# Kernel tuning notes

Hardware: AMD Instinct MI355X
Metric: run time of the kernel (lower is better)

## Reference

```python
import jax, jax.numpy as jnp
import numpy as np

H = 16  # num_heads


def setup_inputs() -> dict:
    key = jax.random.key(0)
    ks = jax.random.split(key, 12)
    b, n, c, T = 4, 1024, 512, 4096

    def lin_w(k, out_d, in_d):
        return jax.random.normal(k, (out_d, in_d), jnp.float32) * (1.0 / np.sqrt(in_d))

    return {
        "feat": jax.random.normal(ks[0], (b, n, c), jnp.float32),
        "member_idx": jax.random.randint(ks[1], (b, n), 0, n),
        "cluster_mask": jnp.ones((b, n), jnp.int32),
        "pe_idx": jax.random.randint(ks[2], (b, n, n), 0, T),
        "global_attn": 1,
        "pre_table": jax.random.normal(ks[3], (T, 5), jnp.float32),
        "q_w": lin_w(ks[4], c, c), "q_b": jnp.zeros((c,), jnp.float32),
        "kv_w": lin_w(ks[5], 2 * c, c), "kv_b": jnp.zeros((2 * c,), jnp.float32),
        "pe_w": lin_w(ks[6], H, 5), "pe_b": jnp.zeros((H,), jnp.float32),
        "blank_k": jax.random.normal(ks[7], (c,), jnp.float32) * 0.2,
        "blank_v": jax.random.normal(ks[8], (c,), jnp.float32) * 0.2,
        "proj_w": lin_w(ks[9], c, c), "proj_b": jnp.zeros((c,), jnp.float32),
    }


def reference(feat, member_idx, cluster_mask, pe_idx, global_attn, pre_table,
              q_w, q_b, kv_w, kv_b, pe_w, pe_b, blank_k, blank_v, proj_w, proj_b):
    # global_attn path only (member_idx / cluster_mask unused in this branch)
    b, n, c = feat.shape
    h = H
    c_ = c // h
    scale = c_ ** -0.5

    q = (feat @ q_w.T + q_b) * scale                      # [b,n,c]
    q = q.reshape(b, n, h, c_).transpose(0, 2, 1, 3)      # [b,h,n,c_]
    kv = (feat @ kv_w.T + kv_b).reshape(b, n, h, 2, c_)
    key = kv[..., 0, :].transpose(0, 2, 1, 3)             # [b,h,n,c_]
    v = kv[..., 1, :].transpose(0, 2, 1, 3)               # [b,h,n,c_]

    attn = jnp.einsum('bhqd,bhkd->bhqk', q, key)          # [b,h,n,n]

    pe_out = pre_table @ pe_w.T + pe_b                    # [T,h]
    pos = pe_out[pe_idx].transpose(0, 3, 1, 2)            # [b,h,n,n]
    attn = attn + pos

    blank = jnp.sum(q * blank_k.reshape(1, h, 1, c_), axis=-1, keepdims=True)  # [b,h,n,1]
    attn = jax.nn.softmax(jnp.concatenate([attn, blank], axis=-1), axis=-1)
    blank_attn = attn[..., -1:]                           # [b,h,n,1]
    attn = attn[..., :-1]                                 # [b,h,n,n]

    out = jnp.einsum('bhqk,bhkd->bhqd', attn, v)          # [b,h,n,c_]
    out = out + blank_attn * blank_v.reshape(1, h, 1, c_)
    out = out.transpose(0, 2, 1, 3).reshape(b, n, c)
    return out @ proj_w.T + proj_b
```

## Files before the change

kernel.cpp:

```cpp
#include <hip/hip_runtime.h>
#include <hip/hip_fp16.h>

typedef __attribute__((ext_vector_type(8))) short short8;
typedef __attribute__((ext_vector_type(8))) __bf16 bf16x8;
typedef __attribute__((ext_vector_type(4))) float f32x4;
typedef __attribute__((ext_vector_type(16))) float f32x16;

#define DEV __device__ __forceinline__

DEV unsigned short f2bf(float f) {
    unsigned int u = __float_as_uint(f);
    return (unsigned short)((u + 0x7FFFu + ((u >> 16) & 1u)) >> 16);
}
DEV float bf2f(unsigned short s) { return __uint_as_float(((unsigned int)s) << 16); }
DEV bf16x8 asbf(short8 v) { return __builtin_bit_cast(bf16x8, v); }

__global__ __launch_bounds__(256) void k_prep(const float* __restrict__ feat,
                                              const float* __restrict__ qw, const float* __restrict__ qb,
                                              const float* __restrict__ kvw, const float* __restrict__ kvb,
                                              const float* __restrict__ pew, const float* __restrict__ peb,
                                              const float* __restrict__ pret, const float* __restrict__ projw,
                                              unsigned short* __restrict__ featb,
                                              unsigned short* __restrict__ wqkv, float* __restrict__ bqkv,
                                              unsigned short* __restrict__ projwb, unsigned short* __restrict__ peG) {
    const float scale = 0.17677669529663687f;
    int i0 = blockIdx.x * 256 + threadIdx.x;
    if (i0 < 262144) {
        const float4* f4 = (const float4*)feat + (size_t)i0 * 2;
        float4 a = f4[0], c = f4[1];
        short8 o;
        o[0] = (short)f2bf(a.x); o[1] = (short)f2bf(a.y);
        o[2] = (short)f2bf(a.z); o[3] = (short)f2bf(a.w);
        o[4] = (short)f2bf(c.x); o[5] = (short)f2bf(c.y);
        o[6] = (short)f2bf(c.z); o[7] = (short)f2bf(c.w);
        ((short8*)featb)[i0] = o;
        return;
    }
    int i = i0 - 262144;
    if (i < 786432) {
        int o = i >> 9, k = i & 511;
        float v = (o < 512) ? qw[(o << 9) + k] * scale : kvw[((o - 512) << 9) + k];
        wqkv[i] = f2bf(v);
    } else if (i < 786432 + 262144) {
        int j = i - 786432;
        projwb[j] = f2bf(projw[j]);
    } else if (i < 786432 + 262144 + 1536) {
        int o = i - (786432 + 262144);
        bqkv[o] = (o < 512) ? qb[o] * scale : kvb[o - 512];
    } else if (i < 786432 + 262144 + 1536 + 65536) {
        int j = i - (786432 + 262144 + 1536);
        int t = j >> 4, h = j & 15;
        float s = peb[h];
#pragma unroll
        for (int u = 0; u < 5; u++) s += pret[t * 5 + u] * pew[h * 5 + u];
        peG[(size_t)(h >> 2) * 16384 + t * 4 + (h & 3)] =
            __builtin_bit_cast(unsigned short, __float2half(s));
    }
}

__global__ __launch_bounds__(256) void k_qkv(const unsigned short* __restrict__ A,
                                             const unsigned short* __restrict__ Bw,
                                             const float* __restrict__ bias,
                                             unsigned short* __restrict__ Qf,
                                             unsigned short* __restrict__ Kf,
                                             unsigned short* __restrict__ Vf) {
    __shared__ __align__(16) unsigned short As[128][72];
    __shared__ __align__(16) unsigned short Bs[64][72];
    int tid = threadIdx.x, lane = tid & 63, wid = tid >> 6;
    int m0 = blockIdx.y * 128, n0 = blockIdx.x * 64;
    int wm = wid >> 1, wn = wid & 1;
    f32x4 acc[4][2] = {};

    for (int k0 = 0; k0 < 512; k0 += 64) {
        {
            int row = tid >> 1, cs = (tid & 1) * 32;
            const short8* src = (const short8*)(A + (size_t)(m0 + row) * 512 + k0 + cs);
            short8* dst = (short8*)(&As[row][cs]);
            dst[0] = src[0]; dst[1] = src[1]; dst[2] = src[2]; dst[3] = src[3];
        }
        {
            int row = tid >> 2, cs = (tid & 3) * 16;
            const short8* src = (const short8*)(Bw + (size_t)(n0 + row) * 512 + k0 + cs);
            short8* dst = (short8*)(&Bs[row][cs]);
            dst[0] = src[0]; dst[1] = src[1];
        }
        __syncthreads();
#pragma unroll
        for (int kk = 0; kk < 64; kk += 32) {
            short8 a[4], b[2];
#pragma unroll
            for (int m = 0; m < 4; m++)
                a[m] = *(const short8*)(&As[wm * 64 + m * 16 + (lane & 15)][kk + ((lane >> 4) << 3)]);
#pragma unroll
            for (int n = 0; n < 2; n++)
                b[n] = *(const short8*)(&Bs[wn * 32 + n * 16 + (lane & 15)][kk + ((lane >> 4) << 3)]);
#pragma unroll
            for (int m = 0; m < 4; m++) {
#pragma unroll
                for (int n = 0; n < 2; n++)
                    acc[m][n] = __builtin_amdgcn_mfma_f32_16x16x32_bf16(asbf(a[m]), asbf(b[n]), acc[m][n], 0, 0, 0);
            }
        }
        __syncthreads();
    }
#pragma unroll
    for (int m = 0; m < 4; m++) {
#pragma unroll
        for (int n = 0; n < 2; n++) {
            int col = n0 + wn * 32 + n * 16 + (lane & 15);
            float bv = bias[col];
#pragma unroll
            for (int r = 0; r < 4; r++) {
                int row = m0 + wm * 64 + m * 16 + ((lane >> 4) << 2) + r;
                float v = acc[m][n][r] + bv;
                unsigned short bb = f2bf(v);
                int batch = row >> 10, nn = row & 1023;
                if (col < 512) {
                    int h = col >> 5, d = col & 31;
                    int bh = (batch << 4) + h;
                    int qt = nn >> 5, q5 = nn & 31;
                    int sub = d >> 4, hi2 = (d >> 3) & 1, j = d & 7;
                    Qf[((((size_t)(bh * 32 + qt) * 2 + sub) * 64) + hi2 * 32 + q5) * 8 + j] = bb;
                } else {
                    int oo = col - 512, h = oo >> 6, rem = oo & 63;
                    int bh = (batch << 4) + h;
                    int kt = nn >> 6, ks = (nn >> 5) & 1;
                    if (rem < 32) {
                        int d = rem, half = d >> 4, hi2 = (d >> 3) & 1, j = d & 7, q5 = nn & 31;
                        Kf[((((size_t)((bh * 16 + kt) * 2 + ks) * 2 + half) * 64) + hi2 * 32 + q5) * 8 + j] = bb;
                    } else {
                        int d = rem - 32, nb = nn & 31;
                        int half = nb >> 4, hi2 = (nb >> 3) & 1, j = nb & 7;
                        Vf[((((size_t)((bh * 16 + kt) * 2 + ks) * 2 + half) * 64) + hi2 * 32 + d) * 8 + j] = bb;
                    }
                }
            }
        }
    }
}

__global__ __launch_bounds__(256, 3) void k_attn(const unsigned short* __restrict__ Qf,
                                                 const unsigned short* __restrict__ Kf,
                                                 const unsigned short* __restrict__ Vf,
                                                 const int* __restrict__ pe_idx,
                                                 const unsigned short* __restrict__ peG,
                                                 const float* __restrict__ blank_k,
                                                 const float* __restrict__ blank_v,
                                                 unsigned short* __restrict__ attnO) {
    __shared__ __align__(8) unsigned short peT4[4096][4];
    __shared__ unsigned short idxT[64][34];
    __shared__ unsigned posS[4096];

    int tid = threadIdx.x, lane = tid & 63, w = tid >> 6;
    int q5 = lane & 31, hi = lane >> 5;
    int bid = blockIdx.x;
    int b = bid & 3, qt = (bid >> 2) & 31, hg = bid >> 7;
    int q0 = qt * 32;
    int head = hg * 4 + w, bh = (b << 4) + head;
    int dwsel = w >> 1, halfsel = w & 1;

    {
        const unsigned short* pg = peG + (size_t)hg * 16384;
#pragma unroll
        for (int j2 = 0; j2 < 16; j2++) {
            int r = tid + 256 * j2;
            *(uint2*)&peT4[r][0] = *(const uint2*)(pg + r * 4);
        }
    }

    int sq = tid >> 3, sk8 = (tid & 7) * 8;
    const int* pib = pe_idx + ((size_t)((b << 10) + q0 + sq)) * 1024 + sk8;

    short8 qf[2];
    float lb_, m_run, l_run;
    f32x16 accO = {};
    const f32x16 zero16 = {};

    {
        const unsigned short* qb_ = Qf + ((size_t)(bh * 32 + qt) * 2) * 512 + lane * 8;
        qf[0] = *(const short8*)(qb_);
        qf[1] = *(const short8*)(qb_ + 512);
        float dot = 0.f;
#pragma unroll
        for (int sub = 0; sub < 2; sub++) {
            const float* bk = blank_k + head * 32 + sub * 16 + hi * 8;
#pragma unroll
            for (int t = 0; t < 8; t++) dot += bf2f((unsigned short)qf[sub][t]) * bk[t];
        }
        dot += __shfl_xor(dot, 32, 64);
        lb_ = dot;
        m_run = dot;
        l_run = 1.0f;
    }

    {
        int4 a0 = *(const int4*)(pib);
        int4 a1 = *(const int4*)(pib + 4);
        idxT[sk8 + 0][sq] = (unsigned short)a0.x; idxT[sk8 + 1][sq] = (unsigned short)a0.y;
        idxT[sk8 + 2][sq] = (unsigned short)a0.z; idxT[sk8 + 3][sq] = (unsigned short)a0.w;
        idxT[sk8 + 4][sq] = (unsigned short)a1.x; idxT[sk8 + 5][sq] = (unsigned short)a1.y;
        idxT[sk8 + 6][sq] = (unsigned short)a1.z; idxT[sk8 + 7][sq] = (unsigned short)a1.w;
    }
    __syncthreads();

    for (int kt = 0; kt < 16; kt++) {
#pragma unroll
        for (int j = 0; j < 8; j++) {
            int el = tid + 256 * j;
            int idx = idxT[el >> 5][el & 31];
            uint2 pv = *(const uint2*)&peT4[idx][0];
            *(uint2*)&posS[el * 2] = pv;
        }
        __syncthreads();

        int4 n0_, n1_;
        if (kt < 15) {
            n0_ = *(const int4*)(pib + (kt + 1) * 64);
            n1_ = *(const int4*)(pib + (kt + 1) * 64 + 4);
        }

        f32x16 st[2];
#pragma unroll
        for (int ks = 0; ks < 2; ks++) {
            const unsigned short* kp = Kf + ((size_t)((bh * 16 + kt) * 2 + ks) * 2) * 512 + lane * 8;
            short8 kf0 = *(const short8*)(kp);
            short8 kf1 = *(const short8*)(kp + 512);
            st[ks] = __builtin_amdgcn_mfma_f32_32x32x16_bf16(asbf(kf0), asbf(qf[0]), zero16, 0, 0, 0);
            st[ks] = __builtin_amdgcn_mfma_f32_32x32x16_bf16(asbf(kf1), asbf(qf[1]), st[ks], 0, 0, 0);
        }
#pragma unroll
        for (int ks = 0; ks < 2; ks++) {
#pragma unroll
            for (int r = 0; r < 16; r++) {
                int kl = (r & 3) + 8 * (r >> 2) + 4 * hi + 32 * ks;
                unsigned pd = posS[(kl * 32 + q5) * 2 + dwsel];
                __half2 h2 = __builtin_bit_cast(__half2, pd);
                st[ks][r] += halfsel ? __high2float(h2) : __low2float(h2);
            }
        }
        float tm[16];
#pragma unroll
        for (int i = 0; i < 16; i++) tm[i] = fmaxf(st[0][i], st[1][i]);
#pragma unroll
        for (int i = 0; i < 8; i++) tm[i] = fmaxf(tm[i], tm[i + 8]);
#pragma unroll
        for (int i = 0; i < 4; i++) tm[i] = fmaxf(tm[i], tm[i + 4]);
        float mx = fmaxf(fmaxf(tm[0], tm[1]), fmaxf(tm[2], tm[3]));
        mx = fmaxf(mx, __shfl_xor(mx, 32, 64));
        if (!__all(mx <= m_run + 8.0f)) {
            float mn = fmaxf(m_run, mx);
            float fac = __expf(m_run - mn);
            m_run = mn;
            l_run *= fac;
#pragma unroll
            for (int r = 0; r < 16; r++) {
                int qrow = (r & 3) + 8 * (r >> 2) + 4 * hi;
                float facr = __shfl(fac, qrow, 64);
                accO[r] *= facr;
            }
        }
#pragma unroll
        for (int ks = 0; ks < 2; ks++)
#pragma unroll
            for (int r = 0; r < 16; r++)
                st[ks][r] = __expf(st[ks][r] - m_run);
        float ts[16];
#pragma unroll
        for (int i = 0; i < 16; i++) ts[i] = st[0][i] + st[1][i];
#pragma unroll
        for (int i = 0; i < 8; i++) ts[i] += ts[i + 8];
#pragma unroll
        for (int i = 0; i < 4; i++) ts[i] += ts[i + 4];
        float sum = (ts[0] + ts[1]) + (ts[2] + ts[3]);
        sum += __shfl_xor(sum, 32, 64);
        l_run += sum;
#pragma unroll
        for (int ks = 0; ks < 2; ks++) {
            unsigned pk_[8];
#pragma unroll
            for (int i = 0; i < 8; i++) {
                float plo = st[ks][2 * i], phi = st[ks][2 * i + 1];
                asm("v_cvt_pk_bf16_f32 %0, %1, %2" : "=v"(pk_[i]) : "v"(plo), "v"(phi));
            }
            asm("v_permlane32_swap_b32 %0, %1" : "+v"(pk_[0]), "+v"(pk_[2]));
            asm("v_permlane32_swap_b32 %0, %1" : "+v"(pk_[1]), "+v"(pk_[3]));
            asm("v_permlane32_swap_b32 %0, %1" : "+v"(pk_[4]), "+v"(pk_[6]));
            asm("v_permlane32_swap_b32 %0, %1" : "+v"(pk_[5]), "+v"(pk_[7]));
            uint4 u0 = {pk_[0], pk_[1], pk_[2], pk_[3]};
            uint4 u1 = {pk_[4], pk_[5], pk_[6], pk_[7]};
            short8 pa0 = __builtin_bit_cast(short8, u0);
            short8 pa1 = __builtin_bit_cast(short8, u1);
            const unsigned short* vp = Vf + ((size_t)((bh * 16 + kt) * 2 + ks) * 2) * 512 + lane * 8;
            short8 vf0 = *(const short8*)(vp);
            short8 vf1 = *(const short8*)(vp + 512);
            accO = __builtin_amdgcn_mfma_f32_32x32x16_bf16(asbf(pa0), asbf(vf0), accO, 0, 0, 0);
            accO = __builtin_amdgcn_mfma_f32_32x32x16_bf16(asbf(pa1), asbf(vf1), accO, 0, 0, 0);
        }
        if (kt < 15) {
            idxT[sk8 + 0][sq] = (unsigned short)n0_.x; idxT[sk8 + 1][sq] = (unsigned short)n0_.y;
            idxT[sk8 + 2][sq] = (unsigned short)n0_.z; idxT[sk8 + 3][sq] = (unsigned short)n0_.w;
            idxT[sk8 + 4][sq] = (unsigned short)n1_.x; idxT[sk8 + 5][sq] = (unsigned short)n1_.y;
            idxT[sk8 + 6][sq] = (unsigned short)n1_.z; idxT[sk8 + 7][sq] = (unsigned short)n1_.w;
        }
        __syncthreads();
    }

    {
        float inv = 1.0f / l_run;
        float bw = __expf(lb_ - m_run) * inv;
        float bv = blank_v[head * 32 + q5];
#pragma unroll
        for (int r = 0; r < 16; r++) {
            int qrow = (r & 3) + 8 * (r >> 2) + 4 * hi;
            float inv_r = __shfl(inv, qrow, 64);
            float bw_r = __shfl(bw, qrow, 64);
            float ov = accO[r] * inv_r + bw_r * bv;
            attnO[((size_t)((b << 10) + q0 + qrow)) * 512 + head * 32 + q5] = f2bf(ov);
        }
    }
}

__global__ __launch_bounds__(256) void k_proj(const unsigned short* __restrict__ A,
                                              const unsigned short* __restrict__ Bw,
                                              const float* __restrict__ bias,
                                              float* __restrict__ out) {
    __shared__ __align__(16) unsigned short As[128][72];
    __shared__ __align__(16) unsigned short Bs[64][72];
    int tid = threadIdx.x, lane = tid & 63, wid = tid >> 6;
    int m0 = blockIdx.y * 128, n0 = blockIdx.x * 64;
    int wm = wid >> 1, wn = wid & 1;
    f32x4 acc[4][2] = {};

    for (int k0 = 0; k0 < 512; k0 += 64) {
        {
            int row = tid >> 1, cs = (tid & 1) * 32;
            const short8* src = (const short8*)(A + (size_t)(m0 + row) * 512 + k0 + cs);
            short8* dst = (short8*)(&As[row][cs]);
            dst[0] = src[0]; dst[1] = src[1]; dst[2] = src[2]; dst[3] = src[3];
        }
        {
            int row = tid >> 2, cs = (tid & 3) * 16;
            const short8* src = (const short8*)(Bw + (size_t)(n0 + row) * 512 + k0 + cs);
            short8* dst = (short8*)(&Bs[row][cs]);
            dst[0] = src[0]; dst[1] = src[1];
        }
        __syncthreads();
#pragma unroll
        for (int kk = 0; kk < 64; kk += 32) {
            short8 a[4], b[2];
#pragma unroll
            for (int m = 0; m < 4; m++)
                a[m] = *(const short8*)(&As[wm * 64 + m * 16 + (lane & 15)][kk + ((lane >> 4) << 3)]);
#pragma unroll
            for (int n = 0; n < 2; n++)
                b[n] = *(const short8*)(&Bs[wn * 32 + n * 16 + (lane & 15)][kk + ((lane >> 4) << 3)]);
#pragma unroll
            for (int m = 0; m < 4; m++) {
#pragma unroll
                for (int n = 0; n < 2; n++)
                    acc[m][n] = __builtin_amdgcn_mfma_f32_16x16x32_bf16(asbf(a[m]), asbf(b[n]), acc[m][n], 0, 0, 0);
            }
        }
        __syncthreads();
    }
#pragma unroll
    for (int m = 0; m < 4; m++) {
#pragma unroll
        for (int n = 0; n < 2; n++) {
            int col = n0 + wn * 32 + n * 16 + (lane & 15);
            float bv = bias[col];
#pragma unroll
            for (int r = 0; r < 4; r++) {
                int row = m0 + wm * 64 + m * 16 + ((lane >> 4) << 2) + r;
                out[(size_t)row * 512 + col] = acc[m][n][r] + bv;
            }
        }
    }
}

extern "C" void kernel_launch(void* const* d_in, const int* in_sizes, int n_in,
                              void* d_out, int out_size, void* d_ws, size_t ws_size,
                              hipStream_t stream) {
    const float* feat    = (const float*)d_in[0];
    const int*   pe_idx  = (const int*)d_in[3];
    const float* pret    = (const float*)d_in[5];
    const float* qw      = (const float*)d_in[6];
    const float* qb      = (const float*)d_in[7];
    const float* kvw     = (const float*)d_in[8];
    const float* kvb     = (const float*)d_in[9];
    const float* pew     = (const float*)d_in[10];
    const float* peb     = (const float*)d_in[11];
    const float* blank_k = (const float*)d_in[12];
    const float* blank_v = (const float*)d_in[13];
    const float* projw   = (const float*)d_in[14];
    const float* projb   = (const float*)d_in[15];

    char* ws = (char*)d_ws;
    unsigned short* featb  = (unsigned short*)(ws);
    unsigned short* wqkv   = (unsigned short*)(ws + 4194304);
    unsigned short* projwb = (unsigned short*)(ws + 5767168);
    float*          bqkv   = (float*)(ws + 6291456);
    unsigned short* peG    = (unsigned short*)(ws + 6297600);
    unsigned short* Qf     = (unsigned short*)(ws + 6428672);
    unsigned short* Kf     = (unsigned short*)(ws + 10622976);
    unsigned short* Vf     = (unsigned short*)(ws + 14817280);
    unsigned short* attnO  = featb;

    k_prep<<<dim3(5382), dim3(256), 0, stream>>>(feat, qw, qb, kvw, kvb, pew, peb, pret, projw,
                                                 featb, wqkv, bqkv, projwb, peG);
    k_qkv<<<dim3(24, 32), dim3(256), 0, stream>>>(featb, wqkv, bqkv, Qf, Kf, Vf);
    k_attn<<<dim3(512), dim3(256), 0, stream>>>(Qf, Kf, Vf, pe_idx, peG, blank_k, blank_v, attnO);
    k_proj<<<dim3(8, 32), dim3(256), 0, stream>>>(attnO, projwb, projb, (float*)d_out);
}
```

Measured before the change: 72.37 us.

## Split attention keys across waves with two heads per block and merge softmax

```diff
diff --git a/kernel.cpp b/kernel.cpp
--- a/kernel.cpp
+++ b/kernel.cpp
@@ -22,7 +22,7 @@
                                               const float* __restrict__ pret, const float* __restrict__ projw,
                                               unsigned short* __restrict__ featb,
                                               unsigned short* __restrict__ wqkv, float* __restrict__ bqkv,
-                                              unsigned short* __restrict__ projwb, unsigned short* __restrict__ peG) {
+                                              unsigned short* __restrict__ projwb, unsigned short* __restrict__ peG2) {
     const float scale = 0.17677669529663687f;
     int i0 = blockIdx.x * 256 + threadIdx.x;
     if (i0 < 262144) {
@@ -53,7 +53,7 @@
         float s = peb[h];
 #pragma unroll
         for (int u = 0; u < 5; u++) s += pret[t * 5 + u] * pew[h * 5 + u];
-        peG[(size_t)(h >> 2) * 16384 + t * 4 + (h & 3)] =
+        peG2[(size_t)(h >> 1) * 8192 + t * 2 + (h & 1)] =
             __builtin_bit_cast(unsigned short, __float2half(s));
     }
 }
@@ -139,37 +139,36 @@
     }
 }
 
-__global__ __launch_bounds__(256, 3) void k_attn(const unsigned short* __restrict__ Qf,
+__global__ __launch_bounds__(256, 4) void k_attn(const unsigned short* __restrict__ Qf,
                                                  const unsigned short* __restrict__ Kf,
                                                  const unsigned short* __restrict__ Vf,
                                                  const int* __restrict__ pe_idx,
-                                                 const unsigned short* __restrict__ peG,
+                                                 const unsigned* __restrict__ peG2,
                                                  const float* __restrict__ blank_k,
                                                  const float* __restrict__ blank_v,
                                                  unsigned short* __restrict__ attnO) {
-    __shared__ __align__(8) unsigned short peT4[4096][4];
-    __shared__ unsigned short idxT[64][34];
-    __shared__ unsigned posS[4096];
+    __shared__ unsigned peT2[4096];
+    __shared__ unsigned posS[128 * 33];
 
     int tid = threadIdx.x, lane = tid & 63, w = tid >> 6;
     int q5 = lane & 31, hi = lane >> 5;
     int bid = blockIdx.x;
-    int b = bid & 3, qt = (bid >> 2) & 31, hg = bid >> 7;
+    int b = bid & 3, qt = (bid >> 2) & 31, hg = (bid >> 7) & 7;
     int q0 = qt * 32;
-    int head = hg * 4 + w, bh = (b << 4) + head;
-    int dwsel = w >> 1, halfsel = w & 1;
+    int hl = w & 1, khalf = w >> 1;
+    int head = hg * 2 + hl, bh = (b << 4) + head;
 
     {
-        const unsigned short* pg = peG + (size_t)hg * 16384;
+        const unsigned* pg = peG2 + (size_t)hg * 4096;
 #pragma unroll
         for (int j2 = 0; j2 < 16; j2++) {
             int r = tid + 256 * j2;
-            *(uint2*)&peT4[r][0] = *(const uint2*)(pg + r * 4);
-        }
-    }
-
-    int sq = tid >> 3, sk8 = (tid & 7) * 8;
-    const int* pib = pe_idx + ((size_t)((b << 10) + q0 + sq)) * 1024 + sk8;
+            peT2[r] = pg[r];
+        }
+    }
+
+    int sq = tid >> 3, kg = tid & 7;
+    const int* pibase = pe_idx + ((size_t)((b << 10) + q0 + sq)) * 1024;
 
     short8 qf[2];
     float lb_, m_run, l_run;
@@ -189,40 +188,43 @@
         }
         dot += __shfl_xor(dot, 32, 64);
         lb_ = dot;
-        m_run = dot;
-        l_run = 1.0f;
-    }
-
-    {
-        int4 a0 = *(const int4*)(pib);
-        int4 a1 = *(const int4*)(pib + 4);
-        idxT[sk8 + 0][sq] = (unsigned short)a0.x; idxT[sk8 + 1][sq] = (unsigned short)a0.y;
-        idxT[sk8 + 2][sq] = (unsigned short)a0.z; idxT[sk8 + 3][sq] = (unsigned short)a0.w;
-        idxT[sk8 + 4][sq] = (unsigned short)a1.x; idxT[sk8 + 5][sq] = (unsigned short)a1.y;
-        idxT[sk8 + 6][sq] = (unsigned short)a1.z; idxT[sk8 + 7][sq] = (unsigned short)a1.w;
+        m_run = (khalf == 0) ? dot : -1e30f;
+        l_run = (khalf == 0) ? 1.0f : 0.0f;
+    }
+
+    int4 id4[4];
+#pragma unroll
+    for (int s = 0; s < 4; s++) {
+        int col = (s < 2) ? (kg * 4 + 32 * s) : (512 + kg * 4 + 32 * (s - 2));
+        id4[s] = *(const int4*)(pibase + col);
     }
     __syncthreads();
 
-    for (int kt = 0; kt < 16; kt++) {
-#pragma unroll
-        for (int j = 0; j < 8; j++) {
-            int el = tid + 256 * j;
-            int idx = idxT[el >> 5][el & 31];
-            uint2 pv = *(const uint2*)&peT4[idx][0];
-            *(uint2*)&posS[el * 2] = pv;
-        }
-        __syncthreads();
-
-        int4 n0_, n1_;
-        if (kt < 15) {
-            n0_ = *(const int4*)(pib + (kt + 1) * 64);
-            n1_ = *(const int4*)(pib + (kt + 1) * 64 + 4);
-        }
-
+    for (int step = 0; step < 8; step++) {
+#pragma unroll
+        for (int s = 0; s < 4; s++) {
+            int kb = kg * 4 + 32 * s;
+            int id_[4] = {id4[s].x, id4[s].y, id4[s].z, id4[s].w};
+#pragma unroll
+            for (int c = 0; c < 4; c++)
+                posS[(kb + c) * 33 + sq] = peT2[id_[c]];
+        }
+        __syncthreads();
+
+        if (step < 7) {
+#pragma unroll
+            for (int s = 0; s < 4; s++) {
+                int col = (s < 2) ? ((step + 1) * 64 + kg * 4 + 32 * s)
+                                  : (512 + (step + 1) * 64 + kg * 4 + 32 * (s - 2));
+                id4[s] = *(const int4*)(pibase + col);
+            }
+        }
+
+        int ktg = khalf * 8 + step;
         f32x16 st[2];
 #pragma unroll
         for (int ks = 0; ks < 2; ks++) {
-            const unsigned short* kp = Kf + ((size_t)((bh * 16 + kt) * 2 + ks) * 2) * 512 + lane * 8;
+            const unsigned short* kp = Kf + ((size_t)((bh * 16 + ktg) * 2 + ks) * 2) * 512 + lane * 8;
             short8 kf0 = *(const short8*)(kp);
             short8 kf1 = *(const short8*)(kp + 512);
             st[ks] = __builtin_amdgcn_mfma_f32_32x32x16_bf16(asbf(kf0), asbf(qf[0]), zero16, 0, 0, 0);
@@ -233,9 +235,9 @@
 #pragma unroll
             for (int r = 0; r < 16; r++) {
                 int kl = (r & 3) + 8 * (r >> 2) + 4 * hi + 32 * ks;
-                unsigned pd = posS[(kl * 32 + q5) * 2 + dwsel];
+                unsigned pd = posS[(khalf * 64 + kl) * 33 + q5];
                 __half2 h2 = __builtin_bit_cast(__half2, pd);
-                st[ks][r] += halfsel ? __high2float(h2) : __low2float(h2);
+                st[ks][r] += hl ? __high2float(h2) : __low2float(h2);
             }
         }
         float tm[16];
@@ -290,31 +292,45 @@
             uint4 u1 = {pk_[4], pk_[5], pk_[6], pk_[7]};
             short8 pa0 = __builtin_bit_cast(short8, u0);
             short8 pa1 = __builtin_bit_cast(short8, u1);
-            const unsigned short* vp = Vf + ((size_t)((bh * 16 + kt) * 2 + ks) * 2) * 512 + lane * 8;
+            const unsigned short* vp = Vf + ((size_t)((bh * 16 + ktg) * 2 + ks) * 2) * 512 + lane * 8;
             short8 vf0 = *(const short8*)(vp);
             short8 vf1 = *(const short8*)(vp + 512);
             accO = __builtin_amdgcn_mfma_f32_32x32x16_bf16(asbf(pa0), asbf(vf0), accO, 0, 0, 0);
             accO = __builtin_amdgcn_mfma_f32_32x32x16_bf16(asbf(pa1), asbf(vf1), accO, 0, 0, 0);
         }
-        if (kt < 15) {
-            idxT[sk8 + 0][sq] = (unsigned short)n0_.x; idxT[sk8 + 1][sq] = (unsigned short)n0_.y;
-            idxT[sk8 + 2][sq] = (unsigned short)n0_.z; idxT[sk8 + 3][sq] = (unsigned short)n0_.w;
-            idxT[sk8 + 4][sq] = (unsigned short)n1_.x; idxT[sk8 + 5][sq] = (unsigned short)n1_.y;
-            idxT[sk8 + 6][sq] = (unsigned short)n1_.z; idxT[sk8 + 7][sq] = (unsigned short)n1_.w;
-        }
-        __syncthreads();
-    }
-
-    {
-        float inv = 1.0f / l_run;
-        float bw = __expf(lb_ - m_run) * inv;
+        __syncthreads();
+    }
+
+    float* fb = (float*)posS;
+    float* mS = fb + 2176;
+    float* lS = mS + 64;
+    if (khalf == 1) {
+#pragma unroll
+        for (int r = 0; r < 16; r++)
+            fb[(hl * 64 + lane) * 17 + r] = accO[r];
+        if (hi == 0) {
+            mS[hl * 32 + q5] = m_run;
+            lS[hl * 32 + q5] = l_run;
+        }
+    }
+    __syncthreads();
+    if (khalf == 0) {
+        float mB = mS[hl * 32 + q5], lB = lS[hl * 32 + q5];
+        float M = fmaxf(m_run, mB);
+        float eA = __expf(m_run - M), eB = __expf(mB - M);
+        float L = l_run * eA + lB * eB;
+        float inv = 1.0f / L;
+        float bw = __expf(lb_ - M) * inv;
         float bv = blank_v[head * 32 + q5];
 #pragma unroll
         for (int r = 0; r < 16; r++) {
             int qrow = (r & 3) + 8 * (r >> 2) + 4 * hi;
+            float eA_r = __shfl(eA, qrow, 64);
+            float eB_r = __shfl(eB, qrow, 64);
             float inv_r = __shfl(inv, qrow, 64);
             float bw_r = __shfl(bw, qrow, 64);
-            float ov = accO[r] * inv_r + bw_r * bv;
+            float accB = fb[(hl * 64 + lane) * 17 + r];
+            float ov = (accO[r] * eA_r + accB * eB_r) * inv_r + bw_r * bv;
             attnO[((size_t)((b << 10) + q0 + qrow)) * 512 + head * 32 + q5] = f2bf(ov);
         }
     }
@@ -400,15 +416,16 @@
     unsigned short* wqkv   = (unsigned short*)(ws + 4194304);
     unsigned short* projwb = (unsigned short*)(ws + 5767168);
     float*          bqkv   = (float*)(ws + 6291456);
-    unsigned short* peG    = (unsigned short*)(ws + 6297600);
+    unsigned short* peG2   = (unsigned short*)(ws + 6297600);
     unsigned short* Qf     = (unsigned short*)(ws + 6428672);
     unsigned short* Kf     = (unsigned short*)(ws + 10622976);
     unsigned short* Vf     = (unsigned short*)(ws + 14817280);
     unsigned short* attnO  = featb;
 
     k_prep<<<dim3(5382), dim3(256), 0, stream>>>(feat, qw, qb, kvw, kvb, pew, peb, pret, projw,
-                                                 featb, wqkv, bqkv, projwb, peG);
+                                                 featb, wqkv, bqkv, projwb, peG2);
     k_qkv<<<dim3(24, 32), dim3(256), 0, stream>>>(featb, wqkv, bqkv, Qf, Kf, Vf);
-    k_attn<<<dim3(512), dim3(256), 0, stream>>>(Qf, Kf, Vf, pe_idx, peG, blank_k, blank_v, attnO);
+    k_attn<<<dim3(1024), dim3(256), 0, stream>>>(Qf, Kf, Vf, pe_idx, (const unsigned*)peG2,
+                                                 blank_k, blank_v, attnO);
     k_proj<<<dim3(8, 32), dim3(256), 0, stream>>>(attnO, projwb, projb, (float*)d_out);
 }
```

After: 71.63 us. No clear change (-1.0%).
